# Kernel optimization log

Hardware: AMD Instinct MI355X
Metric: run time of the kernel (lower is better)

Reference implementation:

```python
import jax, jax.numpy as jnp
import numpy as np
import math

B, S, D, E, K = 8, 4096, 1024, 64, 2
NOISE_STD_CFG = 1.0
GSHARD_W, IMP_W, LOAD_W = 0.0, 1.0, 1.0
LN_EPS = 1e-5


def setup_inputs() -> dict:
    key = jax.random.key(0)
    k1, k2, k3 = jax.random.split(key, 3)
    inputs = jax.random.normal(k1, (B, S, D), dtype=jnp.float32)
    noise = jax.random.normal(k2, (B, S, E), dtype=jnp.float32)  # unit noise, scaled in reference
    # xavier_normal_ with gain=0.01 on a [E, D] Linear weight
    w_std = 0.01 * math.sqrt(2.0 / (D + E))
    W = jax.random.normal(k3, (E, D), dtype=jnp.float32) * w_std
    ln_gamma = jnp.ones((D,), dtype=jnp.float32)
    ln_beta = jnp.zeros((D,), dtype=jnp.float32)
    return {"inputs": inputs, "noise": noise, "ln_gamma": ln_gamma, "ln_beta": ln_beta, "W": W}


def _cv_sq(v, ddof):
    # (std / mean)^2 of a 1-D (or flattened) tensor
    std = jnp.std(v, ddof=ddof)
    return (std / jnp.mean(v)) ** 2


def reference(inputs, noise, ln_gamma, ln_beta, W):
    num_experts = W.shape[0]
    # LayerNorm (fresh params: gamma=1, beta=0, eps=1e-5)
    mu = jnp.mean(inputs, axis=-1, keepdims=True)
    var = jnp.mean(jnp.square(inputs - mu), axis=-1, keepdims=True)
    x = (inputs - mu) * jax.lax.rsqrt(var + LN_EPS) * ln_gamma + ln_beta

    # gate logits [B,S,E], shifted by per-token max for stability
    logits = jnp.einsum('bsd,ed->bse', x, W)
    logits = logits - jnp.max(logits, axis=-1, keepdims=True)
    gates = jax.nn.softmax(logits, axis=-1)

    # importance loss: per batch element, CV^2 of per-expert summed gates (unbiased std)
    imp_per_expert = jnp.sum(gates, axis=1)  # [B, E]
    importance_loss = jnp.mean(
        (jnp.std(imp_per_expert, axis=-1, ddof=1) / jnp.mean(imp_per_expert, axis=-1)) ** 2)

    # noisy logits
    noise_std = max(NOISE_STD_CFG / E, 1e-6)
    logits_noisy = logits + noise_std * noise
    gates_noisy = jax.nn.softmax(logits_noisy, axis=-1)

    # load loss
    topk_vals, _ = jax.lax.top_k(logits_noisy, K)  # [B,S,K]
    threshold = topk_vals[..., -1:]                # k-th largest noisy logit
    z = jnp.clip((threshold - logits) / noise_std, -10.0, 10.0)
    p = 0.5 * (1.0 + jax.lax.erf(z / jnp.float32(math.sqrt(2.0))))
    p_mean = jnp.mean(p, axis=0)                   # [S, E]
    load_loss = _cv_sq(p_mean, ddof=0)

    # gshard loss on noisy gates
    gates_flat = gates_noisy.reshape(-1, num_experts)  # [B*S, E]
    mean_gates = jnp.mean(gates_flat, axis=0)
    top1 = jnp.argmax(gates_flat, axis=-1)
    one_hot = jax.nn.one_hot(top1, num_experts, dtype=gates_flat.dtype)
    mean_top1 = jnp.mean(one_hot, axis=0)
    gshard_loss = jnp.mean(mean_top1 * mean_gates) * (num_experts ** 2)

    aux = GSHARD_W * gshard_loss + IMP_W * importance_loss + LOAD_W * load_loss
    return gates_noisy, aux, gshard_loss, importance_loss, load_loss
```

## Files before the change

### kernel.cpp

```cpp
#include <hip/hip_runtime.h>
#include <hip/hip_bf16.h>
#include <math.h>

#define B_ 8
#define S_ 4096
#define D_ 1024
#define E_ 64
#define NOISE_STD 0.015625f
#define INV_NOISE_STD 64.0f
#define OUT_GATES (B_ * S_ * E_)
#define NBLK 1024

typedef __attribute__((ext_vector_type(8))) short short8;
typedef __attribute__((ext_vector_type(4))) float f32x4;

#define WS_GW   32768
#define WS_BW   32832
#define WS_PART 32896
#define PART_STRIDE 644
#define WS_TOT  (WS_PART + NBLK * PART_STRIDE)
#define N_TOT   642

__device__ __forceinline__ float wave_sum64(float v) {
#pragma unroll
  for (int o = 32; o > 0; o >>= 1) v += __shfl_xor(v, o);
  return v;
}

__global__ void router_prep(const float* __restrict__ W,
                            const float* __restrict__ gamma,
                            const float* __restrict__ beta,
                            float* __restrict__ ws) {
  if (blockIdx.x >= E_) {
    for (int i = threadIdx.x; i < N_TOT; i += 256) ws[WS_TOT + i] = 0.0f;
    return;
  }
  const int e = blockIdx.x;
  unsigned short* wgb = (unsigned short*)ws;
  float gw = 0.0f, bw = 0.0f;
  for (int d = threadIdx.x; d < D_; d += 256) {
    float wv = W[e * D_ + d];
    float pv = gamma[d] * wv;
    union { __hip_bfloat16 h; unsigned short u; } cv;
    cv.h = __float2bfloat16(pv);
    wgb[e * D_ + d] = cv.u;
    gw += __bfloat162float(cv.h);
    bw += beta[d] * wv;
  }
  __shared__ float sred[8];
  gw = wave_sum64(gw);
  bw = wave_sum64(bw);
  const int w = threadIdx.x >> 6, lane = threadIdx.x & 63;
  if (lane == 0) { sred[w] = gw; sred[4 + w] = bw; }
  __syncthreads();
  if (threadIdx.x == 0) {
    ws[WS_GW + e] = sred[0] + sred[1] + sred[2] + sred[3];
    ws[WS_BW + e] = sred[4] + sred[5] + sred[6] + sred[7];
  }
}

__global__ void __launch_bounds__(512, 4)
router_main(const float* __restrict__ X, const float* __restrict__ noise,
            float* __restrict__ out, float* __restrict__ ws) {
  __shared__ __align__(16) float unbuf[4352];
  __shared__ __align__(16) float Lg[2176];
  __shared__ float svs[32], sv2s[32];
  __shared__ float cntl[64];
  __shared__ float red8[8];
  float* gcl = unbuf;
  float* gnl = unbuf + 2176;
  float* pl  = Lg;

  const int t = threadIdx.x;
  const int w = t >> 6, lane = t & 63;
  const int lrow = lane & 15, kh = lane >> 4;
  const int bid = blockIdx.x;
  const int s0 = bid * 4;

  const int r_t = t >> 4, c_t = (t & 15) * 4;
  const int ldso = r_t * 68 + c_t;
  const float* __restrict__ xstage =
      X + ((size_t)(r_t & 7) * S_ + (size_t)(s0 + (r_t >> 3))) * D_ + c_t;

  const int rg = w >> 2, et = w & 3;
  const unsigned short* __restrict__ bp =
      (const unsigned short*)ws + (16 * et + lrow) * D_ + kh * 8;
  const float gwv = ws[WS_GW + 16 * et + lrow];
  const float bwv = ws[WS_BW + 16 * et + lrow];

  const int rr_e = lane >> 4, j_e = lane & 15;
  const int r_e = w * 4 + rr_e;
  const int b_e = r_e & 7, sl_e = r_e >> 3;
  const int s_e = s0 + sl_e;
  const float4 nv =
      *(const float4*)(noise + ((size_t)b_e * S_ + s_e) * E_ + 4 * j_e);

  float4 qx[2];
  short8 qb[2][2];
  qx[0] = *(const float4*)(xstage);
  qx[1] = *(const float4*)(xstage + 64);
  qb[0][0] = *(const short8*)(bp);
  qb[0][1] = *(const short8*)(bp + 32);
  qb[1][0] = *(const short8*)(bp + 64);
  qb[1][1] = *(const short8*)(bp + 96);

  float ssv = 0.0f, ssv2 = 0.0f;
  unbuf[ldso + 0] = qx[0].x; unbuf[ldso + 1] = qx[0].y;
  unbuf[ldso + 2] = qx[0].z; unbuf[ldso + 3] = qx[0].w;
  ssv  += (qx[0].x + qx[0].y) + (qx[0].z + qx[0].w);
  ssv2 = fmaf(qx[0].x, qx[0].x, ssv2); ssv2 = fmaf(qx[0].y, qx[0].y, ssv2);
  ssv2 = fmaf(qx[0].z, qx[0].z, ssv2); ssv2 = fmaf(qx[0].w, qx[0].w, ssv2);

  f32x4 acc = {0.f, 0.f, 0.f, 0.f};

#pragma unroll
  for (int s = 0; s < 16; ++s) {
    __syncthreads();
    if (s + 2 < 16)
      qx[s & 1] = *(const float4*)(xstage + (s + 2) * 64);

    const float* xb = unbuf + (s & 1) * 2176 + (16 * rg + lrow) * 68;
#pragma unroll
    for (int ks = 0; ks < 2; ++ks) {
      float4 a0 = *(const float4*)(xb + ks * 32 + kh * 8);
      float4 a1 = *(const float4*)(xb + ks * 32 + kh * 8 + 4);
      union { short8 s8; __hip_bfloat162 h[4]; } u;
      u.h[0] = __float22bfloat162_rn(make_float2(a0.x, a0.y));
      u.h[1] = __float22bfloat162_rn(make_float2(a0.z, a0.w));
      u.h[2] = __float22bfloat162_rn(make_float2(a1.x, a1.y));
      u.h[3] = __float22bfloat162_rn(make_float2(a1.z, a1.w));
      acc = __builtin_amdgcn_mfma_f32_16x16x32_bf16(u.s8, qb[s & 1][ks],
                                                    acc, 0, 0, 0);
    }
    if (s + 2 < 16) {
      qb[s & 1][0] = *(const short8*)(bp + (s + 2) * 64);
      qb[s & 1][1] = *(const short8*)(bp + (s + 2) * 64 + 32);
    }
    if (s + 1 < 16) {
      float4 wv = qx[(s + 1) & 1];
      float* d = unbuf + ((s + 1) & 1) * 2176 + ldso;
      d[0] = wv.x; d[1] = wv.y; d[2] = wv.z; d[3] = wv.w;
      ssv  += (wv.x + wv.y) + (wv.z + wv.w);
      ssv2 = fmaf(wv.x, wv.x, ssv2); ssv2 = fmaf(wv.y, wv.y, ssv2);
      ssv2 = fmaf(wv.z, wv.z, ssv2); ssv2 = fmaf(wv.w, wv.w, ssv2);
    }
  }

  ssv  += __shfl_xor(ssv, 1);  ssv  += __shfl_xor(ssv, 2);
  ssv  += __shfl_xor(ssv, 4);  ssv  += __shfl_xor(ssv, 8);
  ssv2 += __shfl_xor(ssv2, 1); ssv2 += __shfl_xor(ssv2, 2);
  ssv2 += __shfl_xor(ssv2, 4); ssv2 += __shfl_xor(ssv2, 8);
  if ((t & 15) == 0) { svs[r_t] = ssv; sv2s[r_t] = ssv2; }
  if (t < 64) cntl[t] = 0.0f;
  __syncthreads();

#pragma unroll
  for (int i = 0; i < 4; i++) {
    const int rloc = 16 * rg + kh * 4 + i;
    const float mui = svs[rloc] * (1.0f / (float)D_);
    const float var = sv2s[rloc] * (1.0f / (float)D_) - mui * mui;
    const float rsi = rsqrtf(var + 1e-5f);
    Lg[rloc * 68 + 16 * et + lrow] = rsi * (acc[i] - mui * gwv) + bwv;
  }
  __syncthreads();

  {
    const int r = r_e, b = b_e, s = s_e, j = j_e;
    float4 lv = *(const float4*)(Lg + r * 68 + 4 * j);
    float ln0 = fmaf(NOISE_STD, nv.x, lv.x);
    float ln1 = fmaf(NOISE_STD, nv.y, lv.y);
    float ln2 = fmaf(NOISE_STD, nv.z, lv.z);
    float ln3 = fmaf(NOISE_STD, nv.w, lv.w);

    float m1 = ln0, m2 = -INFINITY;
    m2 = fmaxf(m2, fminf(m1, ln1)); m1 = fmaxf(m1, ln1);
    m2 = fmaxf(m2, fminf(m1, ln2)); m1 = fmaxf(m1, ln2);
    m2 = fmaxf(m2, fminf(m1, ln3)); m1 = fmaxf(m1, ln3);
#pragma unroll
    for (int o = 1; o <= 8; o <<= 1) {
      float o1 = __shfl_xor(m1, o), o2 = __shfl_xor(m2, o);
      m2 = fmaxf(fmaxf(m2, o2), fminf(m1, o1));
      m1 = fmaxf(m1, o1);
    }
    float ec0 = __expf(lv.x - m1), ec1 = __expf(lv.y - m1);
    float ec2 = __expf(lv.z - m1), ec3 = __expf(lv.w - m1);
    float en0 = __expf(ln0 - m1), en1 = __expf(ln1 - m1);
    float en2 = __expf(ln2 - m1), en3 = __expf(ln3 - m1);
    float sg = (ec0 + ec1) + (ec2 + ec3);
    float sn = (en0 + en1) + (en2 + en3);
#pragma unroll
    for (int o = 1; o <= 8; o <<= 1) {
      sg += __shfl_xor(sg, o);
      sn += __shfl_xor(sn, o);
    }
    const float rg_ = 1.0f / sg, rn_ = 1.0f / sn;
    float4 gnv = { en0 * rn_, en1 * rn_, en2 * rn_, en3 * rn_ };
    float4 gcv = { ec0 * rg_, ec1 * rg_, ec2 * rg_, ec3 * rg_ };
    float z0 = fminf(fmaxf((m2 - lv.x) * INV_NOISE_STD, -10.f), 10.f);
    float z1 = fminf(fmaxf((m2 - lv.y) * INV_NOISE_STD, -10.f), 10.f);
    float z2 = fminf(fmaxf((m2 - lv.z) * INV_NOISE_STD, -10.f), 10.f);
    float z3 = fminf(fmaxf((m2 - lv.w) * INV_NOISE_STD, -10.f), 10.f);
    float4 pv = { 0.5f * (1.0f + erff(z0 * 0.70710678118654752f)),
                  0.5f * (1.0f + erff(z1 * 0.70710678118654752f)),
                  0.5f * (1.0f + erff(z2 * 0.70710678118654752f)),
                  0.5f * (1.0f + erff(z3 * 0.70710678118654752f)) };

    *(float4*)(out + ((size_t)b * S_ + s) * E_ + 4 * j) = gnv;
    *(float4*)(gnl + r * 68 + 4 * j) = gnv;
    *(float4*)(gcl + r * 68 + 4 * j) = gcv;
    *(float4*)(pl  + r * 68 + 4 * j) = pv;
    if (ln0 == m1) atomicAdd(&cntl[4 * j + 0], 1.0f);
    if (ln1 == m1) atomicAdd(&cntl[4 * j + 1], 1.0f);
    if (ln2 == m1) atomicAdd(&cntl[4 * j + 2], 1.0f);
    if (ln3 == m1) atomicAdd(&cntl[4 * j + 3], 1.0f);
  }
  __syncthreads();

  float* prt = ws + WS_PART + (size_t)bid * PART_STRIDE;
  {
    const int b0i = t >> 6, e0i = t & 63;
    float v = gcl[(0 * 8 + b0i) * 68 + e0i] + gcl[(1 * 8 + b0i) * 68 + e0i] +
              gcl[(2 * 8 + b0i) * 68 + e0i] + gcl[(3 * 8 + b0i) * 68 + e0i];
    prt[t] = v;
  }
  if (t < 64) {
    float sgn = 0.0f;
#pragma unroll
    for (int r = 0; r < 32; r++) sgn += gnl[r * 68 + t];
    prt[512 + t] = sgn;
  } else if (t < 128) {
    prt[576 + (t - 64)] = cntl[t - 64];
  } else if (t < 384) {
    const int idx = t - 128;
    const int slc = idx >> 6, e = idx & 63;
    float P = 0.0f;
#pragma unroll
    for (int b = 0; b < 8; b++) P += pl[(slc * 8 + b) * 68 + e];
    float c1 = P * 0.125f;
    float c2 = c1 * c1;
    c1 = wave_sum64(c1);
    c2 = wave_sum64(c2);
    if (lane == 0) { red8[(w - 2) * 2] = c1; red8[(w - 2) * 2 + 1] = c2; }
  }
  __syncthreads();
  if (t == 0) {
    prt[640] = (red8[0] + red8[2]) + (red8[4] + red8[6]);
    prt[641] = (red8[1] + red8[3]) + (red8[5] + red8[7]);
  }
}

__global__ void router_reduce(float* __restrict__ ws) {
  const int t = threadIdx.x;
  if (t >= N_TOT) return;
  const int base = blockIdx.x * 32;
  const float* p = ws + WS_PART + (size_t)base * PART_STRIDE + t;
  float acc = 0.0f;
#pragma unroll 8
  for (int i = 0; i < 32; ++i) acc += p[(size_t)i * PART_STRIDE];
  atomicAdd(&ws[WS_TOT + t], acc);
}

__global__ void router_final(const float* __restrict__ ws, float* __restrict__ out) {
  const int lane = threadIdx.x;
  const float* tot = ws + WS_TOT;
  float impsum = 0.0f;
  for (int b = 0; b < B_; ++b) {
    float v = tot[b * 64 + lane];
    float sfull = wave_sum64(v);
    float mean = sfull * (1.0f / 64.0f);
    float d = v - mean;
    float ss = wave_sum64(d * d);
    impsum += (ss / 63.0f) / (mean * mean);
  }
  float importance = impsum * (1.0f / (float)B_);

  const float N = (float)(S_ * E_);
  float meanp = tot[640] / N;
  float varp = tot[641] / N - meanp * meanp;
  float load = varp / (meanp * meanp);

  const float inv_rows = 1.0f / (float)(B_ * S_);
  float te = (tot[576 + lane] * inv_rows) * (tot[512 + lane] * inv_rows);
  float gs = wave_sum64(te) * (float)E_;

  if (lane == 0) {
    out[OUT_GATES + 0] = importance + load;
    out[OUT_GATES + 1] = gs;
    out[OUT_GATES + 2] = importance;
    out[OUT_GATES + 3] = load;
  }
}

extern "C" void kernel_launch(void* const* d_in, const int* in_sizes, int n_in,
                              void* d_out, int out_size, void* d_ws, size_t ws_size,
                              hipStream_t stream) {
  (void)in_sizes; (void)n_in; (void)out_size; (void)ws_size;
  const float* X     = (const float*)d_in[0];
  const float* noise = (const float*)d_in[1];
  const float* gamma = (const float*)d_in[2];
  const float* beta  = (const float*)d_in[3];
  const float* W     = (const float*)d_in[4];
  float* out = (float*)d_out;
  float* ws  = (float*)d_ws;

  router_prep<<<dim3(E_ + 1), dim3(256), 0, stream>>>(W, gamma, beta, ws);
  router_main<<<dim3(NBLK), dim3(512), 0, stream>>>(X, noise, out, ws);
  router_reduce<<<dim3(32), dim3(704), 0, stream>>>(ws);
  router_final<<<dim3(1), dim3(64), 0, stream>>>(ws, out);
}
```

Before: 60.20 us.

## Double K-step per pipeline stage and re-layout LDS staging with odd row stride

Measured after the change: 77.92 us. +29.4%, slower.

```diff
diff --git a/kernel.cpp b/kernel.cpp
--- a/kernel.cpp
+++ b/kernel.cpp
@@ -62,13 +62,13 @@
 __global__ void __launch_bounds__(512, 4)
 router_main(const float* __restrict__ X, const float* __restrict__ noise,
             float* __restrict__ out, float* __restrict__ ws) {
-  __shared__ __align__(16) float unbuf[4352];
-  __shared__ __align__(16) float Lg[2176];
+  __shared__ __align__(16) float unbuf[8448];
   __shared__ float svs[32], sv2s[32];
   __shared__ float cntl[64];
-  __shared__ float red8[8];
+  __shared__ float red8[16];
   float* gcl = unbuf;
   float* gnl = unbuf + 2176;
+  float* Lg  = unbuf + 4352;
   float* pl  = Lg;
 
   const int t = threadIdx.x;
@@ -77,10 +77,11 @@
   const int bid = blockIdx.x;
   const int s0 = bid * 4;
 
-  const int r_t = t >> 4, c_t = (t & 15) * 4;
-  const int ldso = r_t * 68 + c_t;
+  const int r_t = t >> 4, c8 = (t & 15) * 8;
+  const int ksub_t = c8 >> 5, cw = c8 & 31;
+  const int ldso = ksub_t * 1056 + r_t * 33 + cw;
   const float* __restrict__ xstage =
-      X + ((size_t)(r_t & 7) * S_ + (size_t)(s0 + (r_t >> 3))) * D_ + c_t;
+      X + ((size_t)(r_t & 7) * S_ + (size_t)(s0 + (r_t >> 3))) * D_ + c8;
 
   const int rg = w >> 2, et = w & 3;
   const unsigned short* __restrict__ bp =
@@ -95,35 +96,43 @@
   const float4 nv =
       *(const float4*)(noise + ((size_t)b_e * S_ + s_e) * E_ + 4 * j_e);
 
-  float4 qx[2];
-  short8 qb[2][2];
-  qx[0] = *(const float4*)(xstage);
-  qx[1] = *(const float4*)(xstage + 64);
-  qb[0][0] = *(const short8*)(bp);
-  qb[0][1] = *(const short8*)(bp + 32);
-  qb[1][0] = *(const short8*)(bp + 64);
-  qb[1][1] = *(const short8*)(bp + 96);
+  float4 qx[2][2];
+  short8 qb[2][4];
+  qx[0][0] = *(const float4*)(xstage);
+  qx[0][1] = *(const float4*)(xstage + 4);
+  qx[1][0] = *(const float4*)(xstage + 128);
+  qx[1][1] = *(const float4*)(xstage + 132);
+#pragma unroll
+  for (int p = 0; p < 2; p++)
+#pragma unroll
+    for (int ks = 0; ks < 4; ks++)
+      qb[p][ks] = *(const short8*)(bp + p * 128 + ks * 32);
 
   float ssv = 0.0f, ssv2 = 0.0f;
-  unbuf[ldso + 0] = qx[0].x; unbuf[ldso + 1] = qx[0].y;
-  unbuf[ldso + 2] = qx[0].z; unbuf[ldso + 3] = qx[0].w;
-  ssv  += (qx[0].x + qx[0].y) + (qx[0].z + qx[0].w);
-  ssv2 = fmaf(qx[0].x, qx[0].x, ssv2); ssv2 = fmaf(qx[0].y, qx[0].y, ssv2);
-  ssv2 = fmaf(qx[0].z, qx[0].z, ssv2); ssv2 = fmaf(qx[0].w, qx[0].w, ssv2);
+#pragma unroll
+  for (int h = 0; h < 2; h++) {
+    float4 v = qx[0][h];
+    float* d = unbuf + ldso + 4 * h;
+    d[0] = v.x; d[1] = v.y; d[2] = v.z; d[3] = v.w;
+    ssv += (v.x + v.y) + (v.z + v.w);
+    ssv2 = fmaf(v.x, v.x, ssv2); ssv2 = fmaf(v.y, v.y, ssv2);
+    ssv2 = fmaf(v.z, v.z, ssv2); ssv2 = fmaf(v.w, v.w, ssv2);
+  }
 
   f32x4 acc = {0.f, 0.f, 0.f, 0.f};
 
 #pragma unroll
-  for (int s = 0; s < 16; ++s) {
+  for (int s = 0; s < 8; ++s) {
     __syncthreads();
-    if (s + 2 < 16)
-      qx[s & 1] = *(const float4*)(xstage + (s + 2) * 64);
-
-    const float* xb = unbuf + (s & 1) * 2176 + (16 * rg + lrow) * 68;
-#pragma unroll
-    for (int ks = 0; ks < 2; ++ks) {
-      float4 a0 = *(const float4*)(xb + ks * 32 + kh * 8);
-      float4 a1 = *(const float4*)(xb + ks * 32 + kh * 8 + 4);
+    if (s + 2 < 8) {
+      qx[s & 1][0] = *(const float4*)(xstage + (s + 2) * 128);
+      qx[s & 1][1] = *(const float4*)(xstage + (s + 2) * 128 + 4);
+    }
+    const float* xb = unbuf + (s & 1) * 4224 + (16 * rg + lrow) * 33 + kh * 8;
+#pragma unroll
+    for (int ks = 0; ks < 4; ++ks) {
+      float4 a0 = *(const float4*)(xb + ks * 1056);
+      float4 a1 = *(const float4*)(xb + ks * 1056 + 4);
       union { short8 s8; __hip_bfloat162 h[4]; } u;
       u.h[0] = __float22bfloat162_rn(make_float2(a0.x, a0.y));
       u.h[1] = __float22bfloat162_rn(make_float2(a0.z, a0.w));
@@ -132,17 +141,21 @@
       acc = __builtin_amdgcn_mfma_f32_16x16x32_bf16(u.s8, qb[s & 1][ks],
                                                     acc, 0, 0, 0);
     }
-    if (s + 2 < 16) {
-      qb[s & 1][0] = *(const short8*)(bp + (s + 2) * 64);
-      qb[s & 1][1] = *(const short8*)(bp + (s + 2) * 64 + 32);
-    }
-    if (s + 1 < 16) {
-      float4 wv = qx[(s + 1) & 1];
-      float* d = unbuf + ((s + 1) & 1) * 2176 + ldso;
-      d[0] = wv.x; d[1] = wv.y; d[2] = wv.z; d[3] = wv.w;
-      ssv  += (wv.x + wv.y) + (wv.z + wv.w);
-      ssv2 = fmaf(wv.x, wv.x, ssv2); ssv2 = fmaf(wv.y, wv.y, ssv2);
-      ssv2 = fmaf(wv.z, wv.z, ssv2); ssv2 = fmaf(wv.w, wv.w, ssv2);
+    if (s + 2 < 8) {
+#pragma unroll
+      for (int ks = 0; ks < 4; ++ks)
+        qb[s & 1][ks] = *(const short8*)(bp + (s + 2) * 128 + ks * 32);
+    }
+    if (s + 1 < 8) {
+#pragma unroll
+      for (int h = 0; h < 2; h++) {
+        float4 v = qx[(s + 1) & 1][h];
+        float* d = unbuf + ((s + 1) & 1) * 4224 + ldso + 4 * h;
+        d[0] = v.x; d[1] = v.y; d[2] = v.z; d[3] = v.w;
+        ssv += (v.x + v.y) + (v.z + v.w);
+        ssv2 = fmaf(v.x, v.x, ssv2); ssv2 = fmaf(v.y, v.y, ssv2);
+        ssv2 = fmaf(v.z, v.z, ssv2); ssv2 = fmaf(v.w, v.w, ssv2);
+      }
     }
   }
 
@@ -219,8 +232,9 @@
   float* prt = ws + WS_PART + (size_t)bid * PART_STRIDE;
   {
     const int b0i = t >> 6, e0i = t & 63;
-    float v = gcl[(0 * 8 + b0i) * 68 + e0i] + gcl[(1 * 8 + b0i) * 68 + e0i] +
-              gcl[(2 * 8 + b0i) * 68 + e0i] + gcl[(3 * 8 + b0i) * 68 + e0i];
+    float v = 0.0f;
+#pragma unroll
+    for (int sl = 0; sl < 4; sl++) v += gcl[(sl * 8 + b0i) * 68 + e0i];
     prt[t] = v;
   }
   if (t < 64) {
```
